# Performance work log

Measured on AMD Instinct MI355X. Metric: run time of the kernel, lower is better.

Reference implementation:

```python
import jax, jax.numpy as jnp
import numpy as np


def pairwise_distance(x):
    # x: [B,N,F] -> squared euclidean distance matrix [B,N,N]
    sq = jnp.sum(x * x, axis=-1)
    d = sq[:, :, None] + sq[:, None, :] - 2.0 * jnp.einsum('bnd,bmd->bnm', x, x)
    return jnp.maximum(d, 0.0)


def knn_adjacency(dist, k):
    # keep the k nearest neighbors of each point (binary adjacency)
    B, N, _ = dist.shape
    idx = jax.lax.top_k(-dist, k)[1]  # [B,N,k]
    A = jnp.zeros((B, N, N), dist.dtype)
    return A.at[jnp.arange(B)[:, None, None], jnp.arange(N)[None, :, None], idx].set(1.0)


def get_laplacian(A):
    # normalized graph Laplacian L = I - D^{-1/2} A D^{-1/2}
    d = jnp.sum(A, axis=-1)
    dinv = jnp.where(d > 0, 1.0 / jnp.sqrt(jnp.maximum(d, 1e-12)), 0.0)
    An = A * dinv[:, :, None] * dinv[:, None, :]
    return jnp.eye(A.shape[-1], dtype=A.dtype)[None] - An


def cheb_conv(x, L, W, b, K):
    # DenseChebConv: Chebyshev recurrence T0=x, T1=Lx, Tk=2L T_{k-1}-T_{k-2};
    # concat along features then dense projection. x:[B,N,Fin], W:[K*Fin,Fout]
    xs = [x]
    if K > 1:
        xs.append(jnp.einsum('bnm,bmf->bnf', L, x))
    for _ in range(2, K):
        xs.append(2.0 * jnp.einsum('bnm,bmf->bnf', L, xs[-1]) - xs[-2])
    xk = jnp.concatenate(xs, axis=-1)
    return jnp.einsum('bnf,fo->bno', xk, W) + b


def segment_max(out, idx):
    # fused replacement of the per-batch/per-cluster python loops:
    # out:[B,N,F], idx:[B,R,S] -> max-pooled cluster features [B,R,F]
    B = out.shape[0]
    g = out[jnp.arange(B)[:, None, None], idx]  # [B,R,S,F]
    return jnp.max(g, axis=2)


def setup_inputs():
    key = jax.random.key(0)
    ks = jax.random.split(key, 12)
    B, N, R, S, P = 32, 1024, 64, 16, 55
    inp = {}
    inp['x'] = jax.random.normal(ks[0], (B, N, 7), jnp.float32)
    inp['x2'] = jax.random.normal(ks[1], (B, N, 3), jnp.float32)
    inp['laplacian_Reeb'] = jax.random.normal(ks[2], (B, R, R), jnp.float32)
    inp['W1'] = jax.random.normal(ks[3], (3 * 7, 64), jnp.float32) * 0.1
    inp['b1'] = jnp.zeros((64,), jnp.float32)
    inp['W_reeb'] = jax.random.normal(ks[4], (6 * 64, 256), jnp.float32) * 0.05
    inp['b_reeb'] = jnp.zeros((256,), jnp.float32)
    inp['W_fps'] = jax.random.normal(ks[5], (6 * 64, 256), jnp.float32) * 0.05
    inp['b_fps'] = jnp.zeros((256,), jnp.float32)
    inp['fc1_w'] = jax.random.normal(ks[6], (512, 256), jnp.float32) * 0.05
    inp['fc1_b'] = jnp.zeros((256,), jnp.float32)
    inp['fc3_w'] = jax.random.normal(ks[7], (256, 40), jnp.float32) * 0.05
    inp['fc3_b'] = jnp.zeros((40,), jnp.float32)
    inp['sccs'] = jax.random.randint(ks[8], (B, R, S), 0, N)
    inp['sccs_fps'] = jax.random.randint(ks[9], (B, P, N), 0, N)
    inp['k'] = 30
    inp['batch_size'] = B
    inp['num_points'] = N
    return inp


def reference(x, x2, laplacian_Reeb, W1, b1, W_reeb, b_reeb, W_fps, b_fps,
              fc1_w, fc1_b, fc3_w, fc3_b, sccs, sccs_fps, k, batch_size, num_points):
    sg = jax.lax.stop_gradient
    # point-cloud kNN Laplacian (torch.no_grad in original)
    L = sg(get_laplacian(knn_adjacency(pairwise_distance(x), k)))
    out = jax.nn.relu(cheb_conv(x, L, W1, b1, 3))  # [B,N,64]
    reg1 = jnp.sum(jnp.einsum('bnf,bnm,bmg->bfg', out, L, out) ** 2)
    # Reeb-graph segment max pooling (no_grad in original)
    V_reeb = sg(segment_max(out, sccs))  # [B,R,64]
    L_reeb = sg(laplacian_Reeb)
    out_reeb = jax.nn.relu(cheb_conv(V_reeb, L_reeb, W_reeb, b_reeb, 6))  # [B,R,256]
    reg2 = jnp.sum(jnp.einsum('bnf,bnm,bmg->bfg', out_reeb, L_reeb, out_reeb) ** 2)
    # FPS cluster max pooling (no_grad in original)
    V_fps = sg(segment_max(out, sccs_fps))  # [B,55,64]
    L_fps = sg(get_laplacian(pairwise_distance(V_fps)))
    out_fps = jax.nn.relu(cheb_conv(V_fps, L_fps, W_fps, b_fps, 6))  # [B,55,256]
    reg3 = jnp.sum(jnp.einsum('bnf,bnm,bmg->bfg', out_fps, L_fps, out_fps) ** 2)
    feat = jnp.concatenate([jnp.max(out_reeb, axis=1), jnp.max(out_fps, axis=1)], axis=1)  # [B,512]
    h = jax.nn.relu(feat @ fc1_w + fc1_b)
    logits = h @ fc3_w + fc3_b  # [B,40]
    regs = jnp.stack([reg1, reg2, reg3,
                      jnp.sum(fc1_w[:, 0] ** 2), fc1_b[0] ** 2,
                      jnp.sum(fc3_w[:, 0] ** 2), fc3_b[0] ** 2])
    return logits, regs
```

## Files before the change

### kernel.cpp

```cpp
#include <hip/hip_runtime.h>
#include <math.h>

#define BN 32
#define NP 1024
#define KNN 30
#define NR 64
#define NFPS 55

__device__ __forceinline__ float lap_s() {
    const float dv = 1.0f / sqrtf(30.0f);
    return dv * dv;
}

__device__ __forceinline__ float dist7(const float4& xiA, const float4& xiB,
                                       float sqi, const float4& ca, const float4& cb) {
#pragma clang fp contract(off)
    float dot = xiA.x * ca.x;
    dot = fmaf(xiA.y, ca.y, dot);
    dot = fmaf(xiA.z, ca.z, dot);
    dot = fmaf(xiA.w, ca.w, dot);
    dot = fmaf(xiB.x, cb.x, dot);
    dot = fmaf(xiB.y, cb.y, dot);
    dot = fmaf(xiB.z, cb.z, dot);
    float r = sqi + cb.w;
    r = r - 2.f * dot;
    return fmaxf(r, 0.f);
}

__global__ __launch_bounds__(256) void k_knn(const float* __restrict__ x,
                                             int* __restrict__ knn,
                                             float* __restrict__ xs1) {
    __shared__ float xls[NP * 8];
    __shared__ float vals[4 * KNN * 64];
    __shared__ float Tm[4 * 64];
    __shared__ int   Pk[4 * 64];
    int b = blockIdx.x;
    int t = threadIdx.x;
    int ln = t & 63, wv = t >> 6;

    const float* xb = x + (size_t)b * NP * 7;
    for (int q = t; q < NP * 8; q += 256) {
        int r = q >> 3, d = q & 7;
        xls[q] = (d < 7) ? xb[r * 7 + d] : 0.f;
    }
    __syncthreads();
    for (int r = t; r < NP; r += 256) {
        float s = 0.f;
#pragma unroll
        for (int d = 0; d < 7; ++d) { float v = xls[r * 8 + d]; s += v * v; }
        xls[r * 8 + 7] = s;
    }
    __syncthreads();

    int grow = blockIdx.y * 64 + ln;
    float4 xiA = *(const float4*)&xls[grow * 8];
    float4 xiB = *(const float4*)&xls[grow * 8 + 4];
    float sqi = xiB.w;

    float bd[KNN];
#pragma unroll
    for (int q = 0; q < KNN; ++q) bd[q] = __builtin_inff();
    int jbase = wv * 256;
    for (int jc = 0; jc < 256; jc += 4) {
        const float* p = &xls[(jbase + jc) * 8];
        float4 a0 = *(const float4*)(p +  0), b0 = *(const float4*)(p +  4);
        float4 a1 = *(const float4*)(p +  8), b1 = *(const float4*)(p + 12);
        float4 a2 = *(const float4*)(p + 16), b2 = *(const float4*)(p + 20);
        float4 a3 = *(const float4*)(p + 24), b3 = *(const float4*)(p + 28);
        float d0 = dist7(xiA, xiB, sqi, a0, b0);
        float d1 = dist7(xiA, xiB, sqi, a1, b1);
        float d2 = dist7(xiA, xiB, sqi, a2, b2);
        float d3 = dist7(xiA, xiB, sqi, a3, b3);
#pragma unroll
        for (int q = KNN - 1; q >= 1; --q) bd[q] = __builtin_amdgcn_fmed3f(bd[q - 1], d0, bd[q]);
        bd[0] = fminf(bd[0], d0);
#pragma unroll
        for (int q = KNN - 1; q >= 1; --q) bd[q] = __builtin_amdgcn_fmed3f(bd[q - 1], d1, bd[q]);
        bd[0] = fminf(bd[0], d1);
#pragma unroll
        for (int q = KNN - 1; q >= 1; --q) bd[q] = __builtin_amdgcn_fmed3f(bd[q - 1], d2, bd[q]);
        bd[0] = fminf(bd[0], d2);
#pragma unroll
        for (int q = KNN - 1; q >= 1; --q) bd[q] = __builtin_amdgcn_fmed3f(bd[q - 1], d3, bd[q]);
        bd[0] = fminf(bd[0], d3);
    }
#pragma unroll
    for (int q = 0; q < KNN; ++q) vals[wv * (KNN * 64) + q * 64 + ln] = bd[q];
    __syncthreads();

    if (t < 64) {
        const float inf = __builtin_inff();
        float h0 = vals[0 * 1920 + t], n0v = vals[0 * 1920 + 64 + t];
        float h1 = vals[1 * 1920 + t], n1v = vals[1 * 1920 + 64 + t];
        float h2 = vals[2 * 1920 + t], n2v = vals[2 * 1920 + 64 + t];
        float h3 = vals[3 * 1920 + t], n3v = vals[3 * 1920 + 64 + t];
        int p0 = 0, p1 = 0, p2 = 0, p3 = 0;
        float lv0 = inf, lv1 = inf, lv2 = inf, lv3 = inf;
        int r0 = 0, r1 = 0, r2 = 0, r3 = 0;
        for (int s = 0; s < KNN; ++s) {
            float best = h0; int bw = 0;
            if (h1 < best) { best = h1; bw = 1; }
            if (h2 < best) { best = h2; bw = 2; }
            if (h3 < best) { best = h3; bw = 3; }
            if (bw == 0) {
                r0 = (best == lv0) ? r0 + 1 : 1; lv0 = best;
                ++p0; h0 = n0v; n0v = (p0 + 1 < KNN) ? vals[0 * 1920 + (p0 + 1) * 64 + t] : inf;
            } else if (bw == 1) {
                r1 = (best == lv1) ? r1 + 1 : 1; lv1 = best;
                ++p1; h1 = n1v; n1v = (p1 + 1 < KNN) ? vals[1 * 1920 + (p1 + 1) * 64 + t] : inf;
            } else if (bw == 2) {
                r2 = (best == lv2) ? r2 + 1 : 1; lv2 = best;
                ++p2; h2 = n2v; n2v = (p2 + 1 < KNN) ? vals[2 * 1920 + (p2 + 1) * 64 + t] : inf;
            } else {
                r3 = (best == lv3) ? r3 + 1 : 1; lv3 = best;
                ++p3; h3 = n3v; n3v = (p3 + 1 < KNN) ? vals[3 * 1920 + (p3 + 1) * 64 + t] : inf;
            }
        }
        Tm[0 * 64 + t] = lv0; Pk[0 * 64 + t] = 0 | (r0 << 8) | (p0 << 16);
        int bacc = p0;
        Tm[1 * 64 + t] = lv1; Pk[1 * 64 + t] = bacc | (r1 << 8) | (p1 << 16); bacc += p1;
        Tm[2 * 64 + t] = lv2; Pk[2 * 64 + t] = bacc | (r2 << 8) | (p2 << 16); bacc += p2;
        Tm[3 * 64 + t] = lv3; Pk[3 * 64 + t] = bacc | (r3 << 8) | (p3 << 16);
    }
    __syncthreads();

    float Tw = Tm[wv * 64 + ln];
    int pk = Pk[wv * 64 + ln];
    int base = pk & 255, need = (pk >> 8) & 255, tk = pk >> 16;
    int* kout = knn + ((size_t)b * NP + grow) * KNN;
    float n0 = 0.f, n1 = 0.f, n2 = 0.f, n3 = 0.f, n4 = 0.f, n5 = 0.f, n6 = 0.f;
    int cs = 0, ct = 0;
    for (int jc = 0; jc < 256; jc += 4) {
        const float* p = &xls[(jbase + jc) * 8];
        float4 a0 = *(const float4*)(p +  0), b0 = *(const float4*)(p +  4);
        float4 a1 = *(const float4*)(p +  8), b1 = *(const float4*)(p + 12);
        float4 a2 = *(const float4*)(p + 16), b2 = *(const float4*)(p + 20);
        float4 a3 = *(const float4*)(p + 24), b3 = *(const float4*)(p + 28);
        float d0 = dist7(xiA, xiB, sqi, a0, b0);
        float d1 = dist7(xiA, xiB, sqi, a1, b1);
        float d2 = dist7(xiA, xiB, sqi, a2, b2);
        float d3 = dist7(xiA, xiB, sqi, a3, b3);
#pragma unroll
        for (int u = 0; u < 4; ++u) {
            float dist = (u == 0) ? d0 : (u == 1) ? d1 : (u == 2) ? d2 : d3;
            const float4& ca = (u == 0) ? a0 : (u == 1) ? a1 : (u == 2) ? a2 : a3;
            const float4& cb = (u == 0) ? b0 : (u == 1) ? b1 : (u == 2) ? b2 : b3;
            bool lt = dist < Tw;
            bool eq = (dist == Tw) && (ct < need);
            if ((lt || eq) && (cs + ct < tk)) {
                kout[base + cs + ct] = jbase + jc + u;
                cs += lt ? 1 : 0;
                ct += eq ? 1 : 0;
                n0 += ca.x; n1 += ca.y; n2 += ca.z; n3 += ca.w;
                n4 += cb.x; n5 += cb.y; n6 += cb.z;
            }
        }
    }
    for (int q = cs + ct; q < tk; ++q) kout[base + q] = grow;
    float* nsb = vals;
    nsb[wv * 448 + 0 * 64 + ln] = n0;
    nsb[wv * 448 + 1 * 64 + ln] = n1;
    nsb[wv * 448 + 2 * 64 + ln] = n2;
    nsb[wv * 448 + 3 * 64 + ln] = n3;
    nsb[wv * 448 + 4 * 64 + ln] = n4;
    nsb[wv * 448 + 5 * 64 + ln] = n5;
    nsb[wv * 448 + 6 * 64 + ln] = n6;
    __syncthreads();
    for (int u = t; u < 448; u += 256) {
        int d = u >> 6, rl = u & 63;
        float tot = nsb[d * 64 + rl] + nsb[448 + d * 64 + rl]
                  + nsb[896 + d * 64 + rl] + nsb[1344 + d * 64 + rl];
        int gr = blockIdx.y * 64 + rl;
        xs1[((size_t)b * NP + gr) * 7 + d] = xls[gr * 8 + d] - lap_s() * tot;
    }
}

__global__ __launch_bounds__(256) void k_out(const float* __restrict__ x,
                                             const float* __restrict__ xs1,
                                             const int* __restrict__ knn,
                                             const float* __restrict__ W1,
                                             const float* __restrict__ b1,
                                             float* __restrict__ out,
                                             const float* __restrict__ fc1_w,
                                             const float* __restrict__ fc1_b,
                                             const float* __restrict__ fc3_w,
                                             const float* __restrict__ fc3_b,
                                             float* __restrict__ regs,
                                             float* __restrict__ Cbuf) {
    __shared__ float x1s[NP * 7];
    __shared__ float x0s[64 * 7];
    __shared__ float fr[64 * 21];
    __shared__ float W1s[21 * 64];
    __shared__ float b1s[64];
    int b = blockIdx.x, y = blockIdx.y;
    int t = threadIdx.x;
    if (y == 16) {
        float* cb = Cbuf + (size_t)b * 4096;
        for (int q = t; q < 4096; q += 256) cb[q] = 0.f;
        if (b != 0) return;
        float* r1 = x1s;
        float* r2 = x1s + 256;
        float s1 = 0.f;
        for (int i = t; i < 512; i += 256) { float v = fc1_w[(size_t)i * 256]; s1 += v * v; }
        float v2 = fc3_w[(size_t)t * 40];
        r1[t] = s1; r2[t] = v2 * v2;
        __syncthreads();
        for (int st = 128; st > 0; st >>= 1) {
            if (t < st) { r1[t] += r1[t + st]; r2[t] += r2[t + st]; }
            __syncthreads();
        }
        if (t == 0) {
            regs[0] = 0.f; regs[1] = 0.f; regs[2] = 0.f;
            regs[3] = r1[0];
            regs[4] = fc1_b[0] * fc1_b[0];
            regs[5] = r2[0];
            regs[6] = fc3_b[0] * fc3_b[0];
        }
        return;
    }
    int rbase = y * 64;
    for (int q = t; q < NP * 7; q += 256) x1s[q] = xs1[(size_t)b * NP * 7 + q];
    for (int q = t; q < 64 * 7; q += 256) x0s[q] = x[(size_t)b * NP * 7 + (size_t)rbase * 7 + q];
    for (int q = t; q < 21 * 64; q += 256) W1s[q] = W1[q];
    if (t < 64) b1s[t] = b1[t];
    __syncthreads();
    if (t < 64) {
        int i = rbase + t;
        float f[21];
#pragma unroll
        for (int d = 0; d < 7; ++d) { f[d] = x0s[t * 7 + d]; f[7 + d] = x1s[i * 7 + d]; }
        float ns[7] = {0.f, 0.f, 0.f, 0.f, 0.f, 0.f, 0.f};
        const int* kn = knn + ((size_t)b * NP + i) * KNN;
        for (int q = 0; q < KNN; ++q) {
            int j = kn[q];
#pragma unroll
            for (int d = 0; d < 7; ++d) ns[d] += x1s[j * 7 + d];
        }
        const float s = lap_s();
#pragma unroll
        for (int d = 0; d < 7; ++d) f[14 + d] = 2.f * (f[7 + d] - s * ns[d]) - f[d];
#pragma unroll
        for (int d = 0; d < 21; ++d) fr[t * 21 + d] = f[d];
    }
    __syncthreads();
    int o = t & 63, g = t >> 6;
    for (int m = 0; m < 16; ++m) {
        int r = g * 16 + m;
        float acc = b1s[o];
#pragma unroll
        for (int d = 0; d < 21; ++d) acc += fr[r * 21 + d] * W1s[d * 64 + o];
        out[((size_t)b * NP + rbase + r) * 64 + o] = fmaxf(acc, 0.f);
    }
}

__global__ __launch_bounds__(256) void k_z1v(const float* __restrict__ out,
                                             const int* __restrict__ knn,
                                             const int* __restrict__ sccs,
                                             const int* __restrict__ sccs_fps,
                                             float* __restrict__ Z1,
                                             float* __restrict__ Vr,
                                             float* __restrict__ Vf) {
    __shared__ unsigned bmw[32];
    __shared__ float red[256];
    int b = blockIdx.x, y = blockIdx.y;
    int t = threadIdx.x;
    const float* ob = out + (size_t)b * NP * 64;
    if (y < 256) {
        int i = y * 4 + (t >> 6);
        int f = t & 63;
        const int* kn = knn + ((size_t)b * NP + i) * KNN;
        float sum = 0.f;
        for (int q = 0; q < KNN; ++q) sum += ob[(size_t)kn[q] * 64 + f];
        Z1[((size_t)b * NP + i) * 64 + f] = ob[(size_t)i * 64 + f] - lap_s() * sum;
    } else if (y < 272) {
        int r = (y - 256) * 4 + (t >> 6);
        int f = t & 63;
        const int* sc = sccs + ((size_t)b * NR + r) * 16;
        float m = -__builtin_inff();
        for (int q = 0; q < 16; ++q) m = fmaxf(m, ob[(size_t)sc[q] * 64 + f]);
        Vr[((size_t)b * NR + r) * 64 + f] = m;
    } else {
        int p = y - 272;
        const int* sp = sccs_fps + ((size_t)b * NFPS + p) * 1024;
        if (t < 32) bmw[t] = 0u;
        __syncthreads();
        for (int q = t; q < 1024; q += 256) {
            int r = sp[q];
            atomicOr(&bmw[r >> 5], 1u << (r & 31));
        }
        __syncthreads();
        int f = t & 63, sc = t >> 6;
        float m = -__builtin_inff();
        for (int w0 = sc * 8; w0 < sc * 8 + 8; ++w0) {
            unsigned w = bmw[w0];
            while (w) {
                int bit = __ffs(w) - 1;
                w &= w - 1;
                m = fmaxf(m, ob[(size_t)(w0 * 32 + bit) * 64 + f]);
            }
        }
        red[t] = m; __syncthreads();
        if (sc == 0) {
            m = fmaxf(fmaxf(red[f], red[64 + f]), fmaxf(red[128 + f], red[192 + f]));
            Vf[((size_t)b * NFPS + p) * 64 + f] = m;
        }
    }
}

__device__ __forceinline__ void t1_part(const float* __restrict__ out,
                                        const float* __restrict__ Z1,
                                        float* __restrict__ Cbuf,
                                        float* buf, int y) {
    int b = blockIdx.x, t = threadIdx.x;
    float* os = buf;
    float* zs = buf + 8192;
    const float* ob = out + ((size_t)b * NP + (size_t)y * 128) * 64;
    const float* zb = Z1 + ((size_t)b * NP + (size_t)y * 128) * 64;
    for (int q = t; q < 128 * 64; q += 256) { os[q] = ob[q]; zs[q] = zb[q]; }
    __syncthreads();
    int f0 = (t & 15) * 4, g0 = (t >> 4) * 4;
    float4 ac0 = make_float4(0.f, 0.f, 0.f, 0.f);
    float4 ac1 = ac0, ac2 = ac0, ac3 = ac0;
#pragma unroll 4
    for (int n = 0; n < 128; ++n) {
        float4 ov = *(const float4*)&os[n * 64 + f0];
        float4 zv = *(const float4*)&zs[n * 64 + g0];
        ac0.x += ov.x * zv.x; ac0.y += ov.x * zv.y; ac0.z += ov.x * zv.z; ac0.w += ov.x * zv.w;
        ac1.x += ov.y * zv.x; ac1.y += ov.y * zv.y; ac1.z += ov.y * zv.z; ac1.w += ov.y * zv.w;
        ac2.x += ov.z * zv.x; ac2.y += ov.z * zv.y; ac2.z += ov.z * zv.z; ac2.w += ov.z * zv.w;
        ac3.x += ov.w * zv.x; ac3.y += ov.w * zv.y; ac3.z += ov.w * zv.z; ac3.w += ov.w * zv.w;
    }
    float* cb = Cbuf + (size_t)b * 4096;
    atomicAdd(&cb[(f0 + 0) * 64 + g0 + 0], ac0.x);
    atomicAdd(&cb[(f0 + 0) * 64 + g0 + 1], ac0.y);
    atomicAdd(&cb[(f0 + 0) * 64 + g0 + 2], ac0.z);
    atomicAdd(&cb[(f0 + 0) * 64 + g0 + 3], ac0.w);
    atomicAdd(&cb[(f0 + 1) * 64 + g0 + 0], ac1.x);
    atomicAdd(&cb[(f0 + 1) * 64 + g0 + 1], ac1.y);
    atomicAdd(&cb[(f0 + 1) * 64 + g0 + 2], ac1.z);
    atomicAdd(&cb[(f0 + 1) * 64 + g0 + 3], ac1.w);
    atomicAdd(&cb[(f0 + 2) * 64 + g0 + 0], ac2.x);
    atomicAdd(&cb[(f0 + 2) * 64 + g0 + 1], ac2.y);
    atomicAdd(&cb[(f0 + 2) * 64 + g0 + 2], ac2.z);
    atomicAdd(&cb[(f0 + 2) * 64 + g0 + 3], ac2.w);
    atomicAdd(&cb[(f0 + 3) * 64 + g0 + 0], ac3.x);
    atomicAdd(&cb[(f0 + 3) * 64 + g0 + 1], ac3.y);
    atomicAdd(&cb[(f0 + 3) * 64 + g0 + 2], ac3.z);
    atomicAdd(&cb[(f0 + 3) * 64 + g0 + 3], ac3.w);
}

__device__ __forceinline__ void lfps_impl(const float* __restrict__ Vfps,
                                          float* __restrict__ Lf, float* buf) {
    int b = blockIdx.x;
    int t = threadIdx.x;
    float* Vs = buf;
    float* sq = buf + 3520;
    float* dist = buf + 3584;
    float* dinv = buf + 6609;
    for (int q = t; q < NFPS * 64; q += 256) Vs[q] = Vfps[(size_t)b * NFPS * 64 + q];
    __syncthreads();
    if (t < NFPS) {
        float s = 0.f;
        for (int f = 0; f < 64; ++f) { float v = Vs[t * 64 + f]; s += v * v; }
        sq[t] = s;
    }
    __syncthreads();
    for (int q = t; q < NFPS * NFPS; q += 256) {
        int i = q / NFPS, j = q % NFPS;
        float dot = 0.f;
        for (int f = 0; f < 64; ++f) dot += Vs[i * 64 + f] * Vs[j * 64 + f];
        dist[q] = fmaxf(sq[i] + sq[j] - 2.f * dot, 0.f);
    }
    __syncthreads();
    if (t < NFPS) {
        float s = 0.f;
        for (int j = 0; j < NFPS; ++j) s += dist[t * NFPS + j];
        dinv[t] = (s > 0.f) ? 1.0f / sqrtf(fmaxf(s, 1e-12f)) : 0.f;
    }
    __syncthreads();
    for (int q = t; q < NFPS * NFPS; q += 256) {
        int i = q / NFPS, j = q % NFPS;
        Lf[(size_t)b * NFPS * NFPS + q] = ((i == j) ? 1.f : 0.f) - dist[q] * dinv[i] * dinv[j];
    }
}

template<int N>
__device__ __forceinline__ void cheb_impl(const float* __restrict__ L,
                                          const float* __restrict__ V,
                                          const float* __restrict__ W,
                                          const float* __restrict__ bias,
                                          float* __restrict__ out,
                                          float* __restrict__ Z,
                                          float* Ls, float* bA, float* bB, float* Ws,
                                          int b, int sl) {
    constexpr int NPAD = (N + 3) & ~3;
    int t = threadIdx.x;
    int c0 = (t & 15) * 4;
    int r0 = (t >> 4) * 4;

    for (int q = t; q < 64 * 64; q += 256) { Ls[q] = 0.f; bA[q] = 0.f; bB[q] = 0.f; }
    __syncthreads();
    for (int q = t; q < N * N; q += 256) {
        int r = q / N, m = q % N;
        Ls[r * 64 + m] = L[(size_t)b * N * N + q];
    }
    for (int q = t; q < N * 64; q += 256) bA[q] = V[(size_t)b * N * 64 + q];
    {
        const float* Wk = W + sl * 64;
        for (int q = t; q < 64 * 64; q += 256) Ws[q] = Wk[(q >> 6) * 256 + (q & 63)];
    }
    float4 a4[4];
    {
        float4 bv = *(const float4*)&bias[sl * 64 + c0];
#pragma unroll
        for (int i = 0; i < 4; ++i) a4[i] = bv;
    }
    __syncthreads();

    auto accum = [&](const float* xb) {
#pragma unroll 2
        for (int m = 0; m < 64; m += 4) {
            float4 xv[4], wv[4];
#pragma unroll
            for (int i = 0; i < 4; ++i) xv[i] = *(const float4*)&xb[(r0 + i) * 64 + m];
#pragma unroll
            for (int mm = 0; mm < 4; ++mm) wv[mm] = *(const float4*)&Ws[(m + mm) * 64 + c0];
#pragma unroll
            for (int i = 0; i < 4; ++i) {
                float xi0 = xv[i].x, xi1 = xv[i].y, xi2 = xv[i].z, xi3 = xv[i].w;
                a4[i].x += xi0 * wv[0].x; a4[i].y += xi0 * wv[0].y; a4[i].z += xi0 * wv[0].z; a4[i].w += xi0 * wv[0].w;
                a4[i].x += xi1 * wv[1].x; a4[i].y += xi1 * wv[1].y; a4[i].z += xi1 * wv[1].z; a4[i].w += xi1 * wv[1].w;
                a4[i].x += xi2 * wv[2].x; a4[i].y += xi2 * wv[2].y; a4[i].z += xi2 * wv[2].z; a4[i].w += xi2 * wv[2].w;
                a4[i].x += xi3 * wv[3].x; a4[i].y += xi3 * wv[3].y; a4[i].z += xi3 * wv[3].z; a4[i].w += xi3 * wv[3].w;
            }
        }
    };
    auto chebmm = [&](const float* src, float* dst, bool first) {
        float4 acc[4];
#pragma unroll
        for (int i = 0; i < 4; ++i) acc[i] = make_float4(0.f, 0.f, 0.f, 0.f);
#pragma unroll 2
        for (int m = 0; m < NPAD; m += 4) {
            float4 sv[4], lv[4];
#pragma unroll
            for (int mm = 0; mm < 4; ++mm) sv[mm] = *(const float4*)&src[(m + mm) * 64 + c0];
#pragma unroll
            for (int i = 0; i < 4; ++i) lv[i] = *(const float4*)&Ls[(r0 + i) * 64 + m];
#pragma unroll
            for (int i = 0; i < 4; ++i) {
                float l0 = lv[i].x, l1 = lv[i].y, l2 = lv[i].z, l3 = lv[i].w;
                acc[i].x += l0 * sv[0].x; acc[i].y += l0 * sv[0].y; acc[i].z += l0 * sv[0].z; acc[i].w += l0 * sv[0].w;
                acc[i].x += l1 * sv[1].x; acc[i].y += l1 * sv[1].y; acc[i].z += l1 * sv[1].z; acc[i].w += l1 * sv[1].w;
                acc[i].x += l2 * sv[2].x; acc[i].y += l2 * sv[2].y; acc[i].z += l2 * sv[2].z; acc[i].w += l2 * sv[2].w;
                acc[i].x += l3 * sv[3].x; acc[i].y += l3 * sv[3].y; acc[i].z += l3 * sv[3].z; acc[i].w += l3 * sv[3].w;
            }
        }
#pragma unroll
        for (int i = 0; i < 4; ++i) {
            if (r0 + i < N) {
                float4* d = (float4*)&dst[(r0 + i) * 64 + c0];
                if (first) *d = acc[i];
                else {
                    float4 od = *d;
                    *d = make_float4(2.f * acc[i].x - od.x, 2.f * acc[i].y - od.y,
                                     2.f * acc[i].z - od.z, 2.f * acc[i].w - od.w);
                }
            }
        }
    };
    auto loadW = [&](int k) {
        const float* Wk = W + (size_t)k * 64 * 256 + sl * 64;
        for (int q = t; q < 64 * 64; q += 256) Ws[q] = Wk[(q >> 6) * 256 + (q & 63)];
    };

    accum(bA);                 __syncthreads();
    chebmm(bA, bB, true);      loadW(1);  __syncthreads();
    accum(bB);                 __syncthreads();
    chebmm(bB, bA, false);     loadW(2);  __syncthreads();
    accum(bA);                 __syncthreads();
    chebmm(bA, bB, false);     loadW(3);  __syncthreads();
    accum(bB);                 __syncthreads();
    chebmm(bB, bA, false);     loadW(4);  __syncthreads();
    accum(bA);                 __syncthreads();
    chebmm(bA, bB, false);     loadW(5);  __syncthreads();
    accum(bB);                 __syncthreads();

    float* ob = out + (size_t)b * N * 256 + sl * 64;
#pragma unroll
    for (int i = 0; i < 4; ++i) {
        if (r0 + i < N) {
            float4 v = make_float4(fmaxf(a4[i].x, 0.f), fmaxf(a4[i].y, 0.f),
                                   fmaxf(a4[i].z, 0.f), fmaxf(a4[i].w, 0.f));
            *(float4*)&bA[(r0 + i) * 64 + c0] = v;
            *(float4*)&ob[(size_t)(r0 + i) * 256 + c0] = v;
        }
    }
    __syncthreads();
    {
        float4 acc[4];
#pragma unroll
        for (int i = 0; i < 4; ++i) acc[i] = make_float4(0.f, 0.f, 0.f, 0.f);
#pragma unroll 2
        for (int m = 0; m < NPAD; m += 4) {
            float4 sv[4], lv[4];
#pragma unroll
            for (int mm = 0; mm < 4; ++mm) sv[mm] = *(const float4*)&bA[(m + mm) * 64 + c0];
#pragma unroll
            for (int i = 0; i < 4; ++i) lv[i] = *(const float4*)&Ls[(r0 + i) * 64 + m];
#pragma unroll
            for (int i = 0; i < 4; ++i) {
                float l0 = lv[i].x, l1 = lv[i].y, l2 = lv[i].z, l3 = lv[i].w;
                acc[i].x += l0 * sv[0].x; acc[i].y += l0 * sv[0].y; acc[i].z += l0 * sv[0].z; acc[i].w += l0 * sv[0].w;
                acc[i].x += l1 * sv[1].x; acc[i].y += l1 * sv[1].y; acc[i].z += l1 * sv[1].z; acc[i].w += l1 * sv[1].w;
                acc[i].x += l2 * sv[2].x; acc[i].y += l2 * sv[2].y; acc[i].z += l2 * sv[2].z; acc[i].w += l2 * sv[2].w;
                acc[i].x += l3 * sv[3].x; acc[i].y += l3 * sv[3].y; acc[i].z += l3 * sv[3].z; acc[i].w += l3 * sv[3].w;
            }
        }
        float* zb = Z + (size_t)b * N * 256 + sl * 64;
#pragma unroll
        for (int i = 0; i < 4; ++i)
            if (r0 + i < N) *(float4*)&zb[(size_t)(r0 + i) * 256 + c0] = acc[i];
    }
}

template<int N>
__device__ __forceinline__ void treg_impl(const float* __restrict__ out,
                                          const float* __restrict__ Z,
                                          float* __restrict__ reg,
                                          float* zs, float* os, float* red, int y) {
    int b = blockIdx.x;
    int f0 = (y >> 1) * 32;
    int g0 = (y & 1) * 128;
    int t = threadIdx.x;
    for (int q = t; q < N * 128; q += 256) {
        int r = q >> 7, gl = q & 127;
        zs[q] = Z[(size_t)b * N * 256 + r * 256 + g0 + gl];
    }
    for (int q = t; q < N * 32; q += 256) {
        int r = q >> 5, f = q & 31;
        os[q] = out[(size_t)b * N * 256 + r * 256 + f0 + f];
    }
    __syncthreads();
    int fl = t >> 3;
    int gb = (t & 7) * 16;
    float accv[16];
#pragma unroll
    for (int q = 0; q < 16; ++q) accv[q] = 0.f;
    for (int n = 0; n < N; ++n) {
        float a = os[n * 32 + fl];
        const float* zr = zs + n * 128 + gb;
#pragma unroll
        for (int q = 0; q < 16; ++q) accv[q] += a * zr[q];
    }
    float loc = 0.f;
#pragma unroll
    for (int q = 0; q < 16; ++q) loc += accv[q] * accv[q];
    red[t] = loc; __syncthreads();
    for (int st = 128; st > 0; st >>= 1) { if (t < st) red[t] += red[t + st]; __syncthreads(); }
    if (t == 0) atomicAdd(reg, red[0]);
}

__global__ __launch_bounds__(256) void k_mid1(
        const float* __restrict__ out, const float* __restrict__ Z1,
        const float* __restrict__ Vfps, float* __restrict__ Cbuf,
        float* __restrict__ Lf,
        const float* __restrict__ Lr, const float* __restrict__ Vr,
        const float* __restrict__ Wr, const float* __restrict__ br,
        float* __restrict__ outR, float* __restrict__ Zr) {
    __shared__ float smem[16384];
    int y = blockIdx.y;
    if (y < 8)       t1_part(out, Z1, Cbuf, smem, y);
    else if (y == 8) lfps_impl(Vfps, Lf, smem);
    else cheb_impl<NR>(Lr, Vr, Wr, br, outR, Zr,
                       smem, smem + 4096, smem + 8192, smem + 12288,
                       blockIdx.x, y - 9);
}

__global__ __launch_bounds__(256) void k_mid2(
        const float* __restrict__ Lf, const float* __restrict__ Vf,
        const float* __restrict__ Wf, const float* __restrict__ bf,
        float* __restrict__ outP, float* __restrict__ Zf,
        const float* __restrict__ outR, const float* __restrict__ Zr,
        const float* __restrict__ Cbuf, float* __restrict__ regs) {
    __shared__ float smem[16384];
    int y = blockIdx.y;
    if (y < 4) cheb_impl<NFPS>(Lf, Vf, Wf, bf, outP, Zf,
                               smem, smem + 4096, smem + 8192, smem + 12288,
                               blockIdx.x, y);
    else if (y < 20) treg_impl<NR>(outR, Zr, regs + 1, smem, smem + 8192, smem + 10240, y - 4);
    else {
        int b = blockIdx.x, t = threadIdx.x;
        float* red = smem;
        float loc = 0.f;
        for (int q = t; q < 4096; q += 256) { float v = Cbuf[(size_t)b * 4096 + q]; loc += v * v; }
        red[t] = loc; __syncthreads();
        for (int st = 128; st > 0; st >>= 1) { if (t < st) red[t] += red[t + st]; __syncthreads(); }
        if (t == 0) atomicAdd(&regs[0], red[0]);
    }
}

__global__ __launch_bounds__(256) void k_fin(
        const float* __restrict__ outP, const float* __restrict__ Zf,
        const float* __restrict__ outR,
        const float* __restrict__ fc1_w, const float* __restrict__ fc1_b,
        const float* __restrict__ fc3_w, const float* __restrict__ fc3_b,
        float* __restrict__ regs, float* __restrict__ logits) {
    __shared__ float smem[10496];
    int y = blockIdx.y;
    if (y < 16) treg_impl<NFPS>(outP, Zf, regs + 2, smem, smem + 8192, smem + 10240, y);
    else {
        int b = blockIdx.x, t = threadIdx.x;
        float* feat = smem;
        float* h = smem + 8192;
        float m = -__builtin_inff();
        for (int r = 0; r < NR; ++r) m = fmaxf(m, outR[((size_t)b * NR + r) * 256 + t]);
        feat[t] = m;
        m = -__builtin_inff();
        for (int p = 0; p < NFPS; ++p) m = fmaxf(m, outP[((size_t)b * NFPS + p) * 256 + t]);
        feat[256 + t] = m;
        __syncthreads();
        float a = fc1_b[t];
        for (int i = 0; i < 512; ++i) a += feat[i] * fc1_w[(size_t)i * 256 + t];
        h[t] = fmaxf(a, 0.f);
        __syncthreads();
        if (t < 40) {
            float a2 = fc3_b[t];
            for (int i = 0; i < 256; ++i) a2 += h[i] * fc3_w[(size_t)i * 40 + t];
            logits[(size_t)b * 40 + t] = a2;
        }
    }
}

extern "C" void kernel_launch(void* const* d_in, const int* in_sizes, int n_in,
                              void* d_out, int out_size, void* d_ws, size_t ws_size,
                              hipStream_t stream) {
    const float* x      = (const float*)d_in[0];
    const float* L_reeb = (const float*)d_in[2];
    const float* W1     = (const float*)d_in[3];
    const float* b1     = (const float*)d_in[4];
    const float* W_reeb = (const float*)d_in[5];
    const float* b_reeb = (const float*)d_in[6];
    const float* W_fps  = (const float*)d_in[7];
    const float* b_fps  = (const float*)d_in[8];
    const float* fc1_w  = (const float*)d_in[9];
    const float* fc1_b  = (const float*)d_in[10];
    const float* fc3_w  = (const float*)d_in[11];
    const float* fc3_b  = (const float*)d_in[12];
    const int*   sccs   = (const int*)d_in[13];
    const int*   sccs_f = (const int*)d_in[14];

    float* outv = (float*)d_out;
    float* regs = outv + 1280;

    char* w = (char*)d_ws;
    size_t off = 0;
    auto alloc = [&](size_t bytes) { void* p = w + off; off = (off + bytes + 255) & ~(size_t)255; return p; };
    int*   knn   = (int*)  alloc((size_t)BN * NP * KNN * 4);
    float* xs1   = (float*)alloc((size_t)BN * NP * 7 * 4);
    float* outF  = (float*)alloc((size_t)BN * NP * 64 * 4);
    float* Z1    = (float*)alloc((size_t)BN * NP * 64 * 4);
    float* Vreeb = (float*)alloc((size_t)BN * NR * 64 * 4);
    float* outRb = (float*)alloc((size_t)BN * NR * 256 * 4);
    float* Z2    = (float*)alloc((size_t)BN * NR * 256 * 4);
    float* Vfps  = (float*)alloc((size_t)BN * NFPS * 64 * 4);
    float* Lfps  = (float*)alloc((size_t)BN * NFPS * NFPS * 4);
    float* outP  = (float*)alloc((size_t)BN * NFPS * 256 * 4);
    float* Z3    = (float*)alloc((size_t)BN * NFPS * 256 * 4);
    float* Cbuf  = (float*)alloc((size_t)BN * 4096 * 4);

    k_knn<<<dim3(BN, NP / 64), 256, 0, stream>>>(x, knn, xs1);
    k_out<<<dim3(BN, 17), 256, 0, stream>>>(x, xs1, knn, W1, b1, outF,
                                            fc1_w, fc1_b, fc3_w, fc3_b, regs, Cbuf);
    k_z1v<<<dim3(BN, 256 + 16 + NFPS), 256, 0, stream>>>(outF, knn, sccs, sccs_f,
                                                         Z1, Vreeb, Vfps);
    k_mid1<<<dim3(BN, 13), 256, 0, stream>>>(outF, Z1, Vfps, Cbuf, Lfps,
                                             L_reeb, Vreeb, W_reeb, b_reeb, outRb, Z2);
    k_mid2<<<dim3(BN, 21), 256, 0, stream>>>(Lfps, Vfps, W_fps, b_fps, outP, Z3,
                                             outRb, Z2, Cbuf, regs);
    k_fin<<<dim3(BN, 17), 256, 0, stream>>>(outP, Z3, outRb,
                                            fc1_w, fc1_b, fc3_w, fc3_b, regs, outv);
}
```

Before: 362.5 us.

## Split KNN candidate scan across 8 lanes per row with shuffle-based merge

Each query row's candidate scan is now spread over 8 lanes of a wavefront, each covering 128 points, instead of 4 waves covering 256 points. Launching 32 rows per block doubles the grid. The per-lane top-30 lists are merged with a register bitonic network over xor shuffles, and the shared-memory merge by a single wave plus its barriers is removed. The neighbour sums and squared norms are also reduced with shuffles, and the shared-memory layout is padded to avoid bank conflicts. The cost is a large register footprint for the 32-element sort under launch_bounds(256,4), and the points are loaded and normed once per block for twice as many blocks.

```diff
diff --git a/kernel.cpp b/kernel.cpp
--- a/kernel.cpp
+++ b/kernel.cpp
@@ -6,6 +6,8 @@
 #define KNN 30
 #define NR 64
 #define NFPS 55
+
+#define XSLOT(r) ((r) * 8 + ((r) >> 7) * 4)
 
 __device__ __forceinline__ float lap_s() {
     const float dv = 1.0f / sqrtf(30.0f);
@@ -27,42 +29,43 @@
     return fmaxf(r, 0.f);
 }
 
-__global__ __launch_bounds__(256) void k_knn(const float* __restrict__ x,
-                                             int* __restrict__ knn,
-                                             float* __restrict__ xs1) {
-    __shared__ float xls[NP * 8];
-    __shared__ float vals[4 * KNN * 64];
-    __shared__ float Tm[4 * 64];
-    __shared__ int   Pk[4 * 64];
+__global__ __launch_bounds__(256, 4) void k_knn(const float* __restrict__ x,
+                                                int* __restrict__ knn,
+                                                float* __restrict__ xs1) {
+    __shared__ float xls[8224];
     int b = blockIdx.x;
     int t = threadIdx.x;
     int ln = t & 63, wv = t >> 6;
+    int seg = ln & 7;
+    int rl  = ln >> 3;
 
     const float* xb = x + (size_t)b * NP * 7;
-    for (int q = t; q < NP * 8; q += 256) {
+#pragma unroll 4
+    for (int k = 0; k < 32; ++k) {
+        int q = k * 256 + t;
         int r = q >> 3, d = q & 7;
-        xls[q] = (d < 7) ? xb[r * 7 + d] : 0.f;
-    }
-    __syncthreads();
-    for (int r = t; r < NP; r += 256) {
-        float s = 0.f;
-#pragma unroll
-        for (int d = 0; d < 7; ++d) { float v = xls[r * 8 + d]; s += v * v; }
-        xls[r * 8 + 7] = s;
-    }
-    __syncthreads();
-
-    int grow = blockIdx.y * 64 + ln;
-    float4 xiA = *(const float4*)&xls[grow * 8];
-    float4 xiB = *(const float4*)&xls[grow * 8 + 4];
+        float v = (d < 7) ? xb[r * 7 + d] : 0.f;
+        float p2 = v * v;
+        p2 += __shfl_xor(p2, 1);
+        p2 += __shfl_xor(p2, 2);
+        p2 += __shfl_xor(p2, 4);
+        xls[XSLOT(r) + d] = (d < 7) ? v : p2;
+    }
+    __syncthreads();
+
+    int grow = blockIdx.y * 32 + wv * 8 + rl;
+    int gslot = XSLOT(grow);
+    float4 xiA = *(const float4*)&xls[gslot];
+    float4 xiB = *(const float4*)&xls[gslot + 4];
     float sqi = xiB.w;
 
     float bd[KNN];
 #pragma unroll
     for (int q = 0; q < KNN; ++q) bd[q] = __builtin_inff();
-    int jbase = wv * 256;
-    for (int jc = 0; jc < 256; jc += 4) {
-        const float* p = &xls[(jbase + jc) * 8];
+    int jbase = seg * 128;
+    int sbase = XSLOT(jbase);
+    for (int jc = 0; jc < 128; jc += 4) {
+        const float* p = &xls[sbase + jc * 8];
         float4 a0 = *(const float4*)(p +  0), b0 = *(const float4*)(p +  4);
         float4 a1 = *(const float4*)(p +  8), b1 = *(const float4*)(p + 12);
         float4 a2 = *(const float4*)(p + 16), b2 = *(const float4*)(p + 20);
@@ -84,54 +87,69 @@
         for (int q = KNN - 1; q >= 1; --q) bd[q] = __builtin_amdgcn_fmed3f(bd[q - 1], d3, bd[q]);
         bd[0] = fminf(bd[0], d3);
     }
-#pragma unroll
-    for (int q = 0; q < KNN; ++q) vals[wv * (KNN * 64) + q * 64 + ln] = bd[q];
-    __syncthreads();
-
-    if (t < 64) {
-        const float inf = __builtin_inff();
-        float h0 = vals[0 * 1920 + t], n0v = vals[0 * 1920 + 64 + t];
-        float h1 = vals[1 * 1920 + t], n1v = vals[1 * 1920 + 64 + t];
-        float h2 = vals[2 * 1920 + t], n2v = vals[2 * 1920 + 64 + t];
-        float h3 = vals[3 * 1920 + t], n3v = vals[3 * 1920 + 64 + t];
-        int p0 = 0, p1 = 0, p2 = 0, p3 = 0;
-        float lv0 = inf, lv1 = inf, lv2 = inf, lv3 = inf;
-        int r0 = 0, r1 = 0, r2 = 0, r3 = 0;
-        for (int s = 0; s < KNN; ++s) {
-            float best = h0; int bw = 0;
-            if (h1 < best) { best = h1; bw = 1; }
-            if (h2 < best) { best = h2; bw = 2; }
-            if (h3 < best) { best = h3; bw = 3; }
-            if (bw == 0) {
-                r0 = (best == lv0) ? r0 + 1 : 1; lv0 = best;
-                ++p0; h0 = n0v; n0v = (p0 + 1 < KNN) ? vals[0 * 1920 + (p0 + 1) * 64 + t] : inf;
-            } else if (bw == 1) {
-                r1 = (best == lv1) ? r1 + 1 : 1; lv1 = best;
-                ++p1; h1 = n1v; n1v = (p1 + 1 < KNN) ? vals[1 * 1920 + (p1 + 1) * 64 + t] : inf;
-            } else if (bw == 2) {
-                r2 = (best == lv2) ? r2 + 1 : 1; lv2 = best;
-                ++p2; h2 = n2v; n2v = (p2 + 1 < KNN) ? vals[2 * 1920 + (p2 + 1) * 64 + t] : inf;
-            } else {
-                r3 = (best == lv3) ? r3 + 1 : 1; lv3 = best;
-                ++p3; h3 = n3v; n3v = (p3 + 1 < KNN) ? vals[3 * 1920 + (p3 + 1) * 64 + t] : inf;
+
+    float m[32];
+#pragma unroll
+    for (int q = 0; q < KNN; ++q) m[q] = bd[q];
+    m[30] = __builtin_inff(); m[31] = __builtin_inff();
+#pragma unroll
+    for (int lvl = 0; lvl < 3; ++lvl) {
+        int mask = 1 << lvl;
+#pragma unroll
+        for (int q = 0; q < 16; ++q) {
+            float u = __shfl_xor(m[31 - q], mask);
+            float v = __shfl_xor(m[q], mask);
+            float lo = fminf(m[q], u);
+            float hi = fminf(m[31 - q], v);
+            m[q] = lo; m[31 - q] = hi;
+        }
+#pragma unroll
+        for (int d = 16; d >= 1; d >>= 1) {
+#pragma unroll
+            for (int i = 0; i < 32; ++i) {
+                if ((i & d) == 0) {
+                    float a = m[i], c = m[i | d];
+                    m[i] = fminf(a, c);
+                    m[i | d] = fmaxf(a, c);
+                }
             }
         }
-        Tm[0 * 64 + t] = lv0; Pk[0 * 64 + t] = 0 | (r0 << 8) | (p0 << 16);
-        int bacc = p0;
-        Tm[1 * 64 + t] = lv1; Pk[1 * 64 + t] = bacc | (r1 << 8) | (p1 << 16); bacc += p1;
-        Tm[2 * 64 + t] = lv2; Pk[2 * 64 + t] = bacc | (r2 << 8) | (p2 << 16); bacc += p2;
-        Tm[3 * 64 + t] = lv3; Pk[3 * 64 + t] = bacc | (r3 << 8) | (p3 << 16);
-    }
-    __syncthreads();
-
-    float Tw = Tm[wv * 64 + ln];
-    int pk = Pk[wv * 64 + ln];
-    int base = pk & 255, need = (pk >> 8) & 255, tk = pk >> 16;
+    }
+    float T = m[29];
+    int firstT = 0;
+#pragma unroll
+    for (int q = 0; q < KNN; ++q) firstT += (m[q] < T) ? 1 : 0;
+    int need = KNN - firstT;
+    int cnt_lt = 0, cnt_eq = 0;
+#pragma unroll
+    for (int q = 0; q < KNN; ++q) {
+        cnt_lt += (bd[q] < T) ? 1 : 0;
+        cnt_eq += (bd[q] == T) ? 1 : 0;
+    }
+    int lanebase = ln & ~7;
+    int pe = 0;
+#pragma unroll
+    for (int s2 = 0; s2 < 7; ++s2) {
+        int v = __shfl(cnt_eq, lanebase + s2);
+        pe += (s2 < seg) ? v : 0;
+    }
+    int e = need - pe;
+    e = (e < 0) ? 0 : e;
+    e = (e > cnt_eq) ? cnt_eq : e;
+    int tk = cnt_lt + e;
+    int pb = 0;
+#pragma unroll
+    for (int s2 = 0; s2 < 7; ++s2) {
+        int v = __shfl(tk, lanebase + s2);
+        pb += (s2 < seg) ? v : 0;
+    }
+    int base = pb;
+
     int* kout = knn + ((size_t)b * NP + grow) * KNN;
     float n0 = 0.f, n1 = 0.f, n2 = 0.f, n3 = 0.f, n4 = 0.f, n5 = 0.f, n6 = 0.f;
     int cs = 0, ct = 0;
-    for (int jc = 0; jc < 256; jc += 4) {
-        const float* p = &xls[(jbase + jc) * 8];
+    for (int jc = 0; jc < 128; jc += 4) {
+        const float* p = &xls[sbase + jc * 8];
         float4 a0 = *(const float4*)(p +  0), b0 = *(const float4*)(p +  4);
         float4 a1 = *(const float4*)(p +  8), b1 = *(const float4*)(p + 12);
         float4 a2 = *(const float4*)(p + 16), b2 = *(const float4*)(p + 20);
@@ -145,8 +163,8 @@
             float dist = (u == 0) ? d0 : (u == 1) ? d1 : (u == 2) ? d2 : d3;
             const float4& ca = (u == 0) ? a0 : (u == 1) ? a1 : (u == 2) ? a2 : a3;
             const float4& cb = (u == 0) ? b0 : (u == 1) ? b1 : (u == 2) ? b2 : b3;
-            bool lt = dist < Tw;
-            bool eq = (dist == Tw) && (ct < need);
+            bool lt = dist < T;
+            bool eq = (dist == T) && (ct < e);
             if ((lt || eq) && (cs + ct < tk)) {
                 kout[base + cs + ct] = jbase + jc + u;
                 cs += lt ? 1 : 0;
@@ -156,22 +174,20 @@
             }
         }
     }
-    for (int q = cs + ct; q < tk; ++q) kout[base + q] = grow;
-    float* nsb = vals;
-    nsb[wv * 448 + 0 * 64 + ln] = n0;
-    nsb[wv * 448 + 1 * 64 + ln] = n1;
-    nsb[wv * 448 + 2 * 64 + ln] = n2;
-    nsb[wv * 448 + 3 * 64 + ln] = n3;
-    nsb[wv * 448 + 4 * 64 + ln] = n4;
-    nsb[wv * 448 + 5 * 64 + ln] = n5;
-    nsb[wv * 448 + 6 * 64 + ln] = n6;
-    __syncthreads();
-    for (int u = t; u < 448; u += 256) {
-        int d = u >> 6, rl = u & 63;
-        float tot = nsb[d * 64 + rl] + nsb[448 + d * 64 + rl]
-                  + nsb[896 + d * 64 + rl] + nsb[1344 + d * 64 + rl];
-        int gr = blockIdx.y * 64 + rl;
-        xs1[((size_t)b * NP + gr) * 7 + d] = xls[gr * 8 + d] - lap_s() * tot;
+#pragma unroll
+    for (int mask = 1; mask <= 4; mask <<= 1) {
+        n0 += __shfl_xor(n0, mask);
+        n1 += __shfl_xor(n1, mask);
+        n2 += __shfl_xor(n2, mask);
+        n3 += __shfl_xor(n3, mask);
+        n4 += __shfl_xor(n4, mask);
+        n5 += __shfl_xor(n5, mask);
+        n6 += __shfl_xor(n6, mask);
+    }
+    if (seg < 7) {
+        float nv = (seg == 0) ? n0 : (seg == 1) ? n1 : (seg == 2) ? n2 :
+                   (seg == 3) ? n3 : (seg == 4) ? n4 : (seg == 5) ? n5 : n6;
+        xs1[((size_t)b * NP + grow) * 7 + seg] = xls[gslot + seg] - lap_s() * nv;
     }
 }
 
@@ -668,7 +684,7 @@
     float* Z3    = (float*)alloc((size_t)BN * NFPS * 256 * 4);
     float* Cbuf  = (float*)alloc((size_t)BN * 4096 * 4);
 
-    k_knn<<<dim3(BN, NP / 64), 256, 0, stream>>>(x, knn, xs1);
+    k_knn<<<dim3(BN, NP / 32), 256, 0, stream>>>(x, knn, xs1);
     k_out<<<dim3(BN, 17), 256, 0, stream>>>(x, xs1, knn, W1, b1, outF,
                                             fc1_w, fc1_b, fc3_w, fc3_b, regs, Cbuf);
     k_z1v<<<dim3(BN, 256 + 16 + NFPS), 256, 0, stream>>>(outF, knn, sccs, sccs_f,
```

Result: no change. 357.8 us (-1.3%).
